# Kernel optimization log

Measured on AMD Instinct MI355X. Metric: run time of the kernel, lower is better.

## Reference

```python
import jax, jax.numpy as jnp
import numpy as np

SCALING = 32.0 / 16.0  # alpha / rank

def setup_inputs() -> dict:
    key = jax.random.key(0)
    k1, k2, k3, k4, k5 = jax.random.split(key, 5)
    B, S, D_IN, D_OUT, R = 4, 2048, 4096, 4096, 16
    x = jax.random.normal(k1, (B, S, D_IN), dtype=jnp.float32)
    weight_int = jax.random.randint(k2, (D_OUT, D_IN), -128, 128, dtype=jnp.int32)
    weight_scale = jax.random.uniform(k3, (1,), dtype=jnp.float32) * 0.01 + 1e-4
    lora_A = jax.random.normal(k4, (R, D_IN), dtype=jnp.float32) * (1.0 / np.sqrt(D_IN))
    lora_B = jax.random.normal(k5, (D_OUT, R), dtype=jnp.float32) * 0.02
    return {"x": x, "weight_int": weight_int, "weight_scale": weight_scale,
            "lora_A": lora_A, "lora_B": lora_B}

def reference(x, weight_int, weight_scale, lora_A, lora_B):
    # Dequantized base weight: [out, in]
    w = weight_int.astype(jnp.float32) * weight_scale  # broadcast scalar scale
    base = jnp.einsum('bsi,oi->bso', x, w)
    # Low-rank LoRA path: (x @ A^T) @ B^T * scaling
    lora = jnp.einsum('bsr,or->bso', jnp.einsum('bsi,ri->bsr', x, lora_A), lora_B) * SCALING
    return base + lora
```

## Files before the change

### kernel.cpp

```cpp
#include <hip/hip_runtime.h>

constexpr int M = 8192;
constexpr int N = 4096;
constexpr int K = 4096;
constexpr float SCALING = 2.0f;

typedef __bf16 bf16x8 __attribute__((ext_vector_type(8)));
typedef __bf16 bf16x4 __attribute__((ext_vector_type(4)));
typedef float  f32x4  __attribute__((ext_vector_type(4)));

__global__ __launch_bounds__(256) void qlora_cast_x(const float* __restrict__ x,
                                                    __bf16* __restrict__ xb) {
    const size_t i = ((size_t)blockIdx.x * 256 + threadIdx.x) * 8;
    const float4 v0 = *(const float4*)(x + i);
    const float4 v1 = *(const float4*)(x + i + 4);
    bf16x8 o;
    o[0] = (__bf16)v0.x; o[1] = (__bf16)v0.y; o[2] = (__bf16)v0.z; o[3] = (__bf16)v0.w;
    o[4] = (__bf16)v1.x; o[5] = (__bf16)v1.y; o[6] = (__bf16)v1.z; o[7] = (__bf16)v1.w;
    *(bf16x8*)(xb + i) = o;
}

__global__ __launch_bounds__(256) void qlora_prep_w(const int* __restrict__ wi,
                                                    const float* __restrict__ wscale,
                                                    const float* __restrict__ lA,
                                                    const float* __restrict__ lB,
                                                    __bf16* __restrict__ W) {
    const int o = blockIdx.x;
    const float s = wscale[0];
    float b[16];
#pragma unroll
    for (int r = 0; r < 16; ++r) b[r] = lB[o * 16 + r];

#pragma unroll
    for (int it = 0; it < 4; ++it) {
        const int i0 = it * 1024 + threadIdx.x * 4;
        const int4 w4 = *(const int4*)(wi + (size_t)o * K + i0);
        float a0 = 0.f, a1 = 0.f, a2 = 0.f, a3 = 0.f;
#pragma unroll
        for (int r = 0; r < 16; ++r) {
            const float4 a4 = *(const float4*)(lA + r * K + i0);
            a0 += b[r] * a4.x; a1 += b[r] * a4.y;
            a2 += b[r] * a4.z; a3 += b[r] * a4.w;
        }
        bf16x4 v;
        v[0] = (__bf16)((float)w4.x * s + SCALING * a0);
        v[1] = (__bf16)((float)w4.y * s + SCALING * a1);
        v[2] = (__bf16)((float)w4.z * s + SCALING * a2);
        v[3] = (__bf16)((float)w4.w * s + SCALING * a3);
        *(bf16x4*)(W + (size_t)o * K + i0) = v;
    }
}

__device__ __forceinline__ void async16(const __bf16* g, __bf16* l) {
    __builtin_amdgcn_global_load_lds(
        (const __attribute__((address_space(1))) unsigned int*)(unsigned long long)g,
        (__attribute__((address_space(3))) unsigned int*)(unsigned int)(unsigned long long)l,
        16, 0, 0);
}

__global__ __launch_bounds__(256) void qlora_gemm_bt(const __bf16* __restrict__ A,
                                                     const __bf16* __restrict__ B,
                                                     float* __restrict__ C) {
    __shared__ __align__(16) __bf16 As[128 * 64];
    __shared__ __align__(16) __bf16 Bs[128 * 64];

    const int tid  = threadIdx.x;
    const int w    = tid >> 6;
    const int lane = tid & 63;
    const int quad = lane >> 4;
    const int lb   = lane & 15;
    const int wm   = w >> 1;
    const int wn   = w & 1;

    const int r8   = lane >> 3;
    const int slot = lane & 7;
    const int q_sw = (slot ^ r8) * 8;

    const size_t mBase = (size_t)blockIdx.y * 128;
    const size_t nBase = (size_t)blockIdx.x * 128;

    const __bf16* gA[4];
    const __bf16* gB[4];
    __bf16* lA[4];
    __bf16* lB[4];
#pragma unroll
    for (int j = 0; j < 4; ++j) {
        const int rt = w * 4 + j;
        gA[j] = A + (mBase + rt * 8 + r8) * K + q_sw;
        gB[j] = B + (nBase + rt * 8 + r8) * K + q_sw;
        lA[j] = As + rt * 512;
        lB[j] = Bs + rt * 512;
    }

    f32x4 acc[4][4] = {};

    for (int kt = 0; kt < K; kt += 64) {
#pragma unroll
        for (int j = 0; j < 4; ++j) async16(gA[j] + kt, lA[j]);
#pragma unroll
        for (int j = 0; j < 4; ++j) async16(gB[j] + kt, lB[j]);
        __syncthreads();

#pragma unroll
        for (int s = 0; s < 2; ++s) {
            bf16x8 af[4], bfr[4];
#pragma unroll
            for (int t = 0; t < 4; ++t) {
                const int rowA = wm * 64 + t * 16 + lb;
                const int rowB = wn * 64 + t * 16 + lb;
                const int sl   = ((s * 4 + quad) ^ (lb & 7)) * 8;
                af[t]  = *(const bf16x8*)(As + rowA * 64 + sl);
                bfr[t] = *(const bf16x8*)(Bs + rowB * 64 + sl);
            }
#pragma unroll
            for (int tm = 0; tm < 4; ++tm)
#pragma unroll
                for (int tn = 0; tn < 4; ++tn)
                    acc[tm][tn] = __builtin_amdgcn_mfma_f32_16x16x32_bf16(
                        af[tm], bfr[tn], acc[tm][tn], 0, 0, 0);
        }
        __syncthreads();
    }

#pragma unroll
    for (int tm = 0; tm < 4; ++tm) {
        const size_t m0 = mBase + wm * 64 + tm * 16 + quad * 4;
#pragma unroll
        for (int tn = 0; tn < 4; ++tn) {
            const size_t n0 = nBase + wn * 64 + tn * 16 + lb;
            float* p = C + m0 * N + n0;
            p[0 * (size_t)N] = acc[tm][tn][0];
            p[1 * (size_t)N] = acc[tm][tn][1];
            p[2 * (size_t)N] = acc[tm][tn][2];
            p[3 * (size_t)N] = acc[tm][tn][3];
        }
    }
}

extern "C" void kernel_launch(void* const* d_in, const int* in_sizes, int n_in,
                              void* d_out, int out_size, void* d_ws, size_t ws_size,
                              hipStream_t stream) {
    const float* x      = (const float*)d_in[0];
    const int*   wint   = (const int*)d_in[1];
    const float* wscale = (const float*)d_in[2];
    const float* lA     = (const float*)d_in[3];
    const float* lB     = (const float*)d_in[4];
    float* out = (float*)d_out;

    __bf16* Xb = (__bf16*)d_ws;
    __bf16* Wb = (__bf16*)((char*)d_ws + (size_t)M * K * 2);

    qlora_cast_x<<<16384, 256, 0, stream>>>(x, Xb);
    qlora_prep_w<<<4096, 256, 0, stream>>>(wint, wscale, lA, lB, Wb);
    qlora_gemm_bt<<<dim3(N / 128, M / 128), 256, 0, stream>>>(Xb, Wb, out);
}
```

Baseline: 617.7 us.

## Switch base GEMM to int8 MFMA with per-row activation quantization and LoRA epilogue

Activations are quantized to int8 per row (with a per-row scale), and the int32 weights are packed to int8. The main GEMM then runs on int8 MFMA with a K-tile of 128 bytes, so each tile moves half the bytes of the bf16 version at the higher int8 instruction rate. The LoRA path is no longer folded into the weight: a separate kernel computes x·Aᵀ, and the GEMM epilogue applies the scales and adds the rank-16 product with one bf16 MFMA per tile. The cost is that activations are quantized coarsely, and x is read twice by two prep kernels, one of which (the rank-16 projection) has poorly coalesced serial row loops.

```diff
diff --git a/kernel.cpp b/kernel.cpp
--- a/kernel.cpp
+++ b/kernel.cpp
@@ -6,63 +6,104 @@
 constexpr float SCALING = 2.0f;
 
 typedef __bf16 bf16x8 __attribute__((ext_vector_type(8)));
-typedef __bf16 bf16x4 __attribute__((ext_vector_type(4)));
 typedef float  f32x4  __attribute__((ext_vector_type(4)));
-
-__global__ __launch_bounds__(256) void qlora_cast_x(const float* __restrict__ x,
-                                                    __bf16* __restrict__ xb) {
+typedef int    int32x4 __attribute__((ext_vector_type(4)));
+
+__global__ __launch_bounds__(256) void qlora_quant_x(const float* __restrict__ x,
+                                                     char* __restrict__ xq,
+                                                     float* __restrict__ sx) {
+    const int m = blockIdx.x;
+    const int t = threadIdx.x;
+    const float4* row = (const float4*)(x + (size_t)m * K + t * 16);
+    float4 v[4];
+#pragma unroll
+    for (int j = 0; j < 4; ++j) v[j] = row[j];
+
+    float amax = 0.f;
+#pragma unroll
+    for (int j = 0; j < 4; ++j) {
+        amax = fmaxf(amax, fabsf(v[j].x)); amax = fmaxf(amax, fabsf(v[j].y));
+        amax = fmaxf(amax, fabsf(v[j].z)); amax = fmaxf(amax, fabsf(v[j].w));
+    }
+#pragma unroll
+    for (int off = 32; off > 0; off >>= 1)
+        amax = fmaxf(amax, __shfl_xor(amax, off, 64));
+    __shared__ float red[4];
+    if ((t & 63) == 0) red[t >> 6] = amax;
+    __syncthreads();
+    const float rmax = fmaxf(fmaxf(fmaxf(red[0], red[1]), fmaxf(red[2], red[3])), 1e-20f);
+    const float q = 127.0f / rmax;
+    if (t == 0) sx[m] = rmax / 127.0f;
+
+    int32x4 p;
+#pragma unroll
+    for (int j = 0; j < 4; ++j) {
+        const int b0 = __float2int_rn(v[j].x * q) & 0xFF;
+        const int b1 = __float2int_rn(v[j].y * q) & 0xFF;
+        const int b2 = __float2int_rn(v[j].z * q) & 0xFF;
+        const int b3 = __float2int_rn(v[j].w * q) & 0xFF;
+        p[j] = b0 | (b1 << 8) | (b2 << 16) | (b3 << 24);
+    }
+    ((int32x4*)(xq + (size_t)m * K))[t] = p;
+}
+
+__global__ __launch_bounds__(256) void qlora_cast_w(const int* __restrict__ wi,
+                                                    char* __restrict__ wq) {
+    const size_t i = ((size_t)blockIdx.x * 256 + threadIdx.x) * 16;
+    int32x4 p;
+#pragma unroll
+    for (int j = 0; j < 4; ++j) {
+        const int32x4 a = *(const int32x4*)(wi + i + j * 4);
+        p[j] = (a[0] & 0xFF) | ((a[1] & 0xFF) << 8) | ((a[2] & 0xFF) << 16) | ((a[3] & 0xFF) << 24);
+    }
+    *(int32x4*)(wq + i) = p;
+}
+
+__global__ __launch_bounds__(256) void qlora_t2(const float* __restrict__ x,
+                                                const float* __restrict__ lA,
+                                                __bf16* __restrict__ T2) {
+    const int j = threadIdx.x >> 4;
+    const int r = threadIdx.x & 15;
+    const size_t m = (size_t)blockIdx.x * 16 + j;
+    const float4* xr = (const float4*)(x + m * K);
+    const float4* ar = (const float4*)(lA + (size_t)r * K);
+    float acc = 0.f;
+#pragma unroll 4
+    for (int i = 0; i < K / 4; ++i) {
+        const float4 a = xr[i];
+        const float4 b = ar[i];
+        acc += a.x * b.x + a.y * b.y + a.z * b.z + a.w * b.w;
+    }
+    T2[m * 16 + r] = (__bf16)(SCALING * acc);
+}
+
+__global__ __launch_bounds__(256) void qlora_cast_lb(const float* __restrict__ lB,
+                                                     __bf16* __restrict__ lBb) {
     const size_t i = ((size_t)blockIdx.x * 256 + threadIdx.x) * 8;
-    const float4 v0 = *(const float4*)(x + i);
-    const float4 v1 = *(const float4*)(x + i + 4);
+    const float4 v0 = *(const float4*)(lB + i);
+    const float4 v1 = *(const float4*)(lB + i + 4);
     bf16x8 o;
     o[0] = (__bf16)v0.x; o[1] = (__bf16)v0.y; o[2] = (__bf16)v0.z; o[3] = (__bf16)v0.w;
     o[4] = (__bf16)v1.x; o[5] = (__bf16)v1.y; o[6] = (__bf16)v1.z; o[7] = (__bf16)v1.w;
-    *(bf16x8*)(xb + i) = o;
-}
-
-__global__ __launch_bounds__(256) void qlora_prep_w(const int* __restrict__ wi,
-                                                    const float* __restrict__ wscale,
-                                                    const float* __restrict__ lA,
-                                                    const float* __restrict__ lB,
-                                                    __bf16* __restrict__ W) {
-    const int o = blockIdx.x;
-    const float s = wscale[0];
-    float b[16];
-#pragma unroll
-    for (int r = 0; r < 16; ++r) b[r] = lB[o * 16 + r];
-
-#pragma unroll
-    for (int it = 0; it < 4; ++it) {
-        const int i0 = it * 1024 + threadIdx.x * 4;
-        const int4 w4 = *(const int4*)(wi + (size_t)o * K + i0);
-        float a0 = 0.f, a1 = 0.f, a2 = 0.f, a3 = 0.f;
-#pragma unroll
-        for (int r = 0; r < 16; ++r) {
-            const float4 a4 = *(const float4*)(lA + r * K + i0);
-            a0 += b[r] * a4.x; a1 += b[r] * a4.y;
-            a2 += b[r] * a4.z; a3 += b[r] * a4.w;
-        }
-        bf16x4 v;
-        v[0] = (__bf16)((float)w4.x * s + SCALING * a0);
-        v[1] = (__bf16)((float)w4.y * s + SCALING * a1);
-        v[2] = (__bf16)((float)w4.z * s + SCALING * a2);
-        v[3] = (__bf16)((float)w4.w * s + SCALING * a3);
-        *(bf16x4*)(W + (size_t)o * K + i0) = v;
-    }
-}
-
-__device__ __forceinline__ void async16(const __bf16* g, __bf16* l) {
+    *(bf16x8*)(lBb + i) = o;
+}
+
+__device__ __forceinline__ void async16(const char* g, char* l) {
     __builtin_amdgcn_global_load_lds(
         (const __attribute__((address_space(1))) unsigned int*)(unsigned long long)g,
         (__attribute__((address_space(3))) unsigned int*)(unsigned int)(unsigned long long)l,
         16, 0, 0);
 }
 
-__global__ __launch_bounds__(256) void qlora_gemm_bt(const __bf16* __restrict__ A,
-                                                     const __bf16* __restrict__ B,
+__global__ __launch_bounds__(256) void qlora_gemm_i8(const char* __restrict__ Aq,
+                                                     const char* __restrict__ Wq,
+                                                     const float* __restrict__ sx,
+                                                     const float* __restrict__ wscale,
+                                                     const __bf16* __restrict__ T2,
+                                                     const __bf16* __restrict__ lBb,
                                                      float* __restrict__ C) {
-    __shared__ __align__(16) __bf16 As[128 * 64];
-    __shared__ __align__(16) __bf16 Bs[128 * 64];
+    __shared__ __align__(16) char As[128 * 128];
+    __shared__ __align__(16) char Bs[128 * 128];
 
     const int tid  = threadIdx.x;
     const int w    = tid >> 6;
@@ -74,27 +115,25 @@
 
     const int r8   = lane >> 3;
     const int slot = lane & 7;
-    const int q_sw = (slot ^ r8) * 8;
+    const int q_sw = ((slot ^ r8) * 16);
 
     const size_t mBase = (size_t)blockIdx.y * 128;
     const size_t nBase = (size_t)blockIdx.x * 128;
 
-    const __bf16* gA[4];
-    const __bf16* gB[4];
-    __bf16* lA[4];
-    __bf16* lB[4];
+    const char* gA[4]; const char* gB[4];
+    char* lA[4]; char* lB[4];
 #pragma unroll
     for (int j = 0; j < 4; ++j) {
         const int rt = w * 4 + j;
-        gA[j] = A + (mBase + rt * 8 + r8) * K + q_sw;
-        gB[j] = B + (nBase + rt * 8 + r8) * K + q_sw;
-        lA[j] = As + rt * 512;
-        lB[j] = Bs + rt * 512;
-    }
-
-    f32x4 acc[4][4] = {};
-
-    for (int kt = 0; kt < K; kt += 64) {
+        gA[j] = Aq + (mBase + rt * 8 + r8) * K + q_sw;
+        gB[j] = Wq + (nBase + rt * 8 + r8) * K + q_sw;
+        lA[j] = As + rt * 1024;
+        lB[j] = Bs + rt * 1024;
+    }
+
+    int32x4 acc[4][4] = {};
+
+    for (int kt = 0; kt < K; kt += 128) {
 #pragma unroll
         for (int j = 0; j < 4; ++j) async16(gA[j] + kt, lA[j]);
 #pragma unroll
@@ -103,36 +142,74 @@
 
 #pragma unroll
         for (int s = 0; s < 2; ++s) {
-            bf16x8 af[4], bfr[4];
+            int32x4 af[4], bfr[4];
 #pragma unroll
             for (int t = 0; t < 4; ++t) {
                 const int rowA = wm * 64 + t * 16 + lb;
                 const int rowB = wn * 64 + t * 16 + lb;
-                const int sl   = ((s * 4 + quad) ^ (lb & 7)) * 8;
-                af[t]  = *(const bf16x8*)(As + rowA * 64 + sl);
-                bfr[t] = *(const bf16x8*)(Bs + rowB * 64 + sl);
+                const int sl   = (((s * 4 + quad) ^ (lb & 7)) * 16);
+                af[t]  = *(const int32x4*)(As + rowA * 128 + sl);
+                bfr[t] = *(const int32x4*)(Bs + rowB * 128 + sl);
             }
 #pragma unroll
             for (int tm = 0; tm < 4; ++tm)
 #pragma unroll
                 for (int tn = 0; tn < 4; ++tn)
-                    acc[tm][tn] = __builtin_amdgcn_mfma_f32_16x16x32_bf16(
+                    acc[tm][tn] = __builtin_amdgcn_mfma_i32_16x16x64_i8(
                         af[tm], bfr[tn], acc[tm][tn], 0, 0, 0);
         }
         __syncthreads();
     }
 
+    {
+        char* epi = As;
+        const int row = tid;
+        const int32x4 z = {0, 0, 0, 0};
+        *(int32x4*)(epi + row * 64 + 32) = z;
+        *(int32x4*)(epi + row * 64 + 48) = z;
+        const char* src = (row < 128)
+            ? ((const char*)T2  + (mBase + row) * 32)
+            : ((const char*)lBb + (nBase + row - 128) * 32);
+        *(int32x4*)(epi + row * 64)      = *(const int32x4*)(src);
+        *(int32x4*)(epi + row * 64 + 16) = *(const int32x4*)(src + 16);
+        float* sxs = (float*)Bs;
+        if (tid < 128) sxs[tid] = sx[mBase + tid];
+    }
+    __syncthreads();
+
+    const float wsv = wscale[0];
+    const float* sxs = (const float*)Bs;
+    const char*  epi = As;
+
+    bf16x8 lbf[4];
+#pragma unroll
+    for (int tn = 0; tn < 4; ++tn) {
+        const int nl = wn * 64 + tn * 16 + lb;
+        lbf[tn] = *(const bf16x8*)(epi + (128 + nl) * 64 + quad * 16);
+    }
+
 #pragma unroll
     for (int tm = 0; tm < 4; ++tm) {
+        const int ml = wm * 64 + tm * 16 + lb;
+        const bf16x8 taf = *(const bf16x8*)(epi + ml * 64 + quad * 16);
+        float sc[4];
+#pragma unroll
+        for (int j = 0; j < 4; ++j) sc[j] = sxs[wm * 64 + tm * 16 + quad * 4 + j] * wsv;
+
         const size_t m0 = mBase + wm * 64 + tm * 16 + quad * 4;
 #pragma unroll
         for (int tn = 0; tn < 4; ++tn) {
+            f32x4 fac;
+#pragma unroll
+            for (int j = 0; j < 4; ++j) fac[j] = (float)acc[tm][tn][j] * sc[j];
+            fac = __builtin_amdgcn_mfma_f32_16x16x32_bf16(taf, lbf[tn], fac, 0, 0, 0);
+
             const size_t n0 = nBase + wn * 64 + tn * 16 + lb;
             float* p = C + m0 * N + n0;
-            p[0 * (size_t)N] = acc[tm][tn][0];
-            p[1 * (size_t)N] = acc[tm][tn][1];
-            p[2 * (size_t)N] = acc[tm][tn][2];
-            p[3 * (size_t)N] = acc[tm][tn][3];
+            p[0 * (size_t)N] = fac[0];
+            p[1 * (size_t)N] = fac[1];
+            p[2 * (size_t)N] = fac[2];
+            p[3 * (size_t)N] = fac[3];
         }
     }
 }
@@ -147,10 +224,16 @@
     const float* lB     = (const float*)d_in[4];
     float* out = (float*)d_out;
 
-    __bf16* Xb = (__bf16*)d_ws;
-    __bf16* Wb = (__bf16*)((char*)d_ws + (size_t)M * K * 2);
-
-    qlora_cast_x<<<16384, 256, 0, stream>>>(x, Xb);
-    qlora_prep_w<<<4096, 256, 0, stream>>>(wint, wscale, lA, lB, Wb);
-    qlora_gemm_bt<<<dim3(N / 128, M / 128), 256, 0, stream>>>(Xb, Wb, out);
-}
+    char* ws = (char*)d_ws;
+    char*    Xq  = ws;
+    char*    Wq  = ws + (size_t)M * K;
+    float*   Sx  = (float*)(ws + (size_t)(M + N) * K);
+    __bf16*  T2  = (__bf16*)(ws + (size_t)(M + N) * K + 32768);
+    __bf16*  LBb = (__bf16*)(ws + (size_t)(M + N) * K + 32768 + 262144);
+
+    qlora_quant_x<<<M, 256, 0, stream>>>(x, Xq, Sx);
+    qlora_cast_w<<<(size_t)N * K / (256 * 16), 256, 0, stream>>>(wint, Wq);
+    qlora_t2<<<M / 16, 256, 0, stream>>>(x, lA, T2);
+    qlora_cast_lb<<<N * 16 / (256 * 8), 256, 0, stream>>>(lB, LBb);
+    qlora_gemm_i8<<<dim3(N / 128, M / 128), 256, 0, stream>>>(Xq, Wq, Sx, wscale, T2, LBb, out);
+}
```

New measurement: 715.3 us. 15.8% more time.
